# Optimization experiments

Hardware: AMD Instinct MI355X
Metric: run time of the kernel (lower is better)

## Reference

```python
import jax, jax.numpy as jnp
import numpy as np

VOCAB = 21128; EMBED = 768; D_MODEL = 256; H = 100; NTAGS = 21; B = 32; T = 256


def setup_inputs() -> dict:
    key = jax.random.key(0)
    ks = jax.random.split(key, 18)
    n = lambda k, s, sc=0.05: jax.random.normal(k, s, dtype=jnp.float32) * sc
    return {
        "words": jax.random.randint(ks[0], (B, T), 0, VOCAB),
        "target": jax.random.randint(ks[1], (B, T), 0, NTAGS),
        "embed_table": n(ks[2], (VOCAB, EMBED), 1.0),
        "in_fc_w": n(ks[3], (D_MODEL, EMBED)),
        "in_fc_b": n(ks[4], (D_MODEL,)),
        "Wih0": n(ks[5], (2, 4 * H, D_MODEL)),
        "Whh0": n(ks[6], (2, 4 * H, H)),
        "bih0": n(ks[7], (2, 4 * H)),
        "bhh0": n(ks[8], (2, 4 * H)),
        "Wih1": n(ks[9], (2, 4 * H, 2 * H)),
        "Whh1": n(ks[10], (2, 4 * H, H)),
        "bih1": n(ks[11], (2, 4 * H)),
        "bhh1": n(ks[12], (2, 4 * H)),
        "out_w": n(ks[13], (NTAGS, 2 * H)),
        "out_b": n(ks[14], (NTAGS,)),
        "trans": n(ks[15], (NTAGS, NTAGS)),
        "start_s": n(ks[16], (NTAGS,)),
        "end_s": n(ks[17], (NTAGS,)),
    }


def _lstm_dir(x, Wih, Whh, bih, bhh, reverse):
    # x: (T, B, D); torch LSTM gate order i, f, g, o
    Bsz, Hd = x.shape[1], Whh.shape[1]
    pre = jnp.einsum('tbd,gd->tbg', x, Wih) + bih  # precompute input projection

    def step(carry, p):
        h, c = carry
        g = p + h @ Whh.T + bhh
        i, f, gg, o = jnp.split(g, 4, axis=-1)
        c = jax.nn.sigmoid(f) * c + jax.nn.sigmoid(i) * jnp.tanh(gg)
        h = jax.nn.sigmoid(o) * jnp.tanh(c)
        return (h, c), h

    init = (jnp.zeros((Bsz, Hd), x.dtype), jnp.zeros((Bsz, Hd), x.dtype))
    _, hs = jax.lax.scan(step, init, pre, reverse=reverse)
    return hs


def _bilstm(x, layers):
    h = x
    for (Wih, Whh, bih, bhh) in layers:  # fixed small loop over num_layers
        f = _lstm_dir(h, Wih[0], Whh[0], bih[0], bhh[0], False)
        b = _lstm_dir(h, Wih[1], Whh[1], bih[1], bhh[1], True)
        h = jnp.concatenate([f, b], axis=-1)
    return h


def _crf_loss(logits, tags, mask, trans, start_s, end_s):
    # fastNLP ConditionalRandomField loss: normalizer - gold_score, per batch elem
    lt = jnp.swapaxes(logits, 0, 1)          # (T, B, N)
    tt = tags.T                               # (T, B)
    mt = mask.T.astype(logits.dtype)          # (T, B)
    alpha0 = lt[0] + start_s

    def step(alpha, inp):
        emit, m = inp
        tmp = alpha[:, :, None] + trans[None] + emit[:, None, :]  # (B, N, N)
        new = jax.nn.logsumexp(tmp, axis=1)
        return jnp.where(m[:, None] > 0, new, alpha), None

    alpha, _ = jax.lax.scan(step, alpha0, (lt[1:], mt[1:]))
    normalizer = jax.nn.logsumexp(alpha + end_s, axis=1)  # (B,)

    emit_sc = jnp.take_along_axis(lt, tt[..., None], axis=2)[..., 0] * mt
    trans_sc = trans[tt[:-1], tt[1:]] * mt[1:]
    seq_lens = mask.sum(axis=1)
    last_idx = jnp.maximum(seq_lens - 1, 0)
    last_tags = tags[jnp.arange(tags.shape[0]), last_idx]
    gold = emit_sc.sum(0) + trans_sc.sum(0) + start_s[tt[0]] + end_s[last_tags]
    return normalizer - gold


def reference(words, target, embed_table, in_fc_w, in_fc_b, Wih0, Whh0, bih0, bhh0,
              Wih1, Whh1, bih1, bhh1, out_w, out_b, trans, start_s, end_s):
    mask = words != 0
    x = embed_table[words]                       # (B, T, E)
    x = x @ in_fc_w.T + in_fc_b                  # (B, T, D)
    x = jnp.swapaxes(x, 0, 1)                    # (T, B, D)
    h = _bilstm(x, [(Wih0, Whh0, bih0, bhh0), (Wih1, Whh1, bih1, bhh1)])
    h = jnp.swapaxes(h, 0, 1)                    # (B, T, 2H); dropout is identity at eval
    logits = jax.nn.log_softmax(h @ out_w.T + out_b, axis=-1)
    return _crf_loss(logits, target, mask, trans, start_s, end_s)  # (B,)
```

## Files before the change

### kernel.cpp

```cpp
#include <hip/hip_runtime.h>
#include <hip/hip_bf16.h>

#define VOCAB 21128
#define EMBED 768
#define DMODEL 256
#define HID 100
#define NTAGS 21
#define BB 32
#define TT 256
#define NTOK (BB*TT)

typedef float f32x4 __attribute__((ext_vector_type(4)));
typedef unsigned int u32x4 __attribute__((ext_vector_type(4)));
typedef short s16x8 __attribute__((ext_vector_type(8)));

__device__ __forceinline__ float sigm(float x) { return 1.0f / (1.0f + __expf(-x)); }
__device__ __forceinline__ float tanh_(float x) { return 2.0f / (1.0f + __expf(-2.0f * x)) - 1.0f; }

__device__ __forceinline__ unsigned int bfr(float x) {
    unsigned int u = __float_as_uint(x);
    return (u + 0x7fffu + ((u >> 16) & 1u)) >> 16;
}
__device__ __forceinline__ unsigned int bfpack(float lo, float hi) {
    return (bfr(hi) << 16) | bfr(lo);
}
__device__ __forceinline__ s16x8 asfrag(u32x4 v) {
    union { u32x4 u; s16x8 s; } x; x.u = v; return x.s;
}

#define BAR() do { \
    asm volatile("s_waitcnt lgkmcnt(0)" ::: "memory"); \
    __builtin_amdgcn_s_barrier(); \
    __builtin_amdgcn_sched_barrier(0); \
} while (0)

__global__ __launch_bounds__(256) void gemm_mfma(
    const float* __restrict__ A, int lda,
    const float* __restrict__ B, int ldb,
    const float* __restrict__ bias1, const float* __restrict__ bias2,
    float* __restrict__ C, int ldc,
    int N, int K,
    const int* __restrict__ gatherWords, int permGates)
{
    __shared__ unsigned int As_[2][4096];
    __shared__ unsigned int Bs_[2][2048];

    const int tid = threadIdx.x;
    const int row0 = blockIdx.x * 128;
    const int col0 = blockIdx.y * 64;
    const int lane = tid & 63;
    const int wave = tid >> 6;
    const int wr = wave >> 1, wc = wave & 1;
    const int nsteps = (K + 63) >> 6;

    const float* arow[8]; int aoff[8]; int kqA[8];
    #pragma unroll
    for (int j = 0; j < 8; ++j) {
        int v = tid + 256 * j;
        int row = v >> 4, kq = v & 15;
        int grow = row0 + row;
        const float* ap;
        if (gatherWords) {
            int widx = gatherWords[(grow & 31) * TT + (grow >> 5)];
            ap = A + (size_t)widx * lda;
        } else {
            ap = A + (size_t)grow * lda;
        }
        arow[j] = ap + 4 * kq;
        aoff[j] = (row >> 4) * 512 + (kq >> 3) * 256 + ((kq >> 1) & 3) * 64
                + (row & 15) * 4 + (kq & 1) * 2;
        kqA[j] = kq;
    }
    const float* brow[4]; int boff[4]; int bok[4]; int kqB[4];
    #pragma unroll
    for (int j = 0; j < 4; ++j) {
        int v = tid + 256 * j;
        int r = v >> 4, kq = v & 15;
        int gcol = col0 + r;
        bok[j] = (gcol < N);
        int src = bok[j] ? gcol : 0;
        if (permGates && bok[j]) {
            int d2 = (gcol >= 400) ? 1 : 0;
            int rr = gcol - d2 * 400;
            src = d2 * 400 + (rr & 3) * 100 + (rr >> 2);
        }
        brow[j] = B + (size_t)src * ldb + 4 * kq;
        boff[j] = (r >> 4) * 512 + (kq >> 3) * 256 + ((kq >> 1) & 3) * 64
                + (r & 15) * 4 + (kq & 1) * 2;
        kqB[j] = kq;
    }

    {
        #pragma unroll
        for (int j = 0; j < 8; ++j) {
            f32x4 v = {0.f,0.f,0.f,0.f};
            if (4 * kqA[j] < K) v = *(const f32x4*)(arow[j]);
            As_[0][aoff[j]]     = bfpack(v.x, v.y);
            As_[0][aoff[j] + 1] = bfpack(v.z, v.w);
        }
        #pragma unroll
        for (int j = 0; j < 4; ++j) {
            f32x4 v = {0.f,0.f,0.f,0.f};
            if (bok[j] && 4 * kqB[j] < K) v = *(const f32x4*)(brow[j]);
            Bs_[0][boff[j]]     = bfpack(v.x, v.y);
            Bs_[0][boff[j] + 1] = bfpack(v.z, v.w);
        }
    }
    BAR();

    f32x4 acc[4][2] = {};

    for (int s = 0; s < nsteps; ++s) {
        const int cur = s & 1, nxt = cur ^ 1;

        f32x4 la[8], lb[4];
        if (s + 1 < nsteps) {
            const int kb = (s + 1) * 64;
            #pragma unroll
            for (int j = 0; j < 8; ++j) {
                la[j] = (f32x4){0.f,0.f,0.f,0.f};
                if (kb + 4 * kqA[j] < K) la[j] = *(const f32x4*)(arow[j] + kb);
            }
            #pragma unroll
            for (int j = 0; j < 4; ++j) {
                lb[j] = (f32x4){0.f,0.f,0.f,0.f};
                if (bok[j] && kb + 4 * kqB[j] < K) lb[j] = *(const f32x4*)(brow[j] + kb);
            }
        }

        u32x4 af[2][4], bf2[2][2];
        #pragma unroll
        for (int f = 0; f < 2; ++f) {
            #pragma unroll
            for (int mt = 0; mt < 4; ++mt)
                af[f][mt] = *(const u32x4*)&As_[cur][(4 * wr + mt) * 512 + f * 256 + lane * 4];
            #pragma unroll
            for (int nt = 0; nt < 2; ++nt)
                bf2[f][nt] = *(const u32x4*)&Bs_[cur][(2 * wc + nt) * 512 + f * 256 + lane * 4];
        }
        #pragma unroll
        for (int f = 0; f < 2; ++f)
            #pragma unroll
            for (int mt = 0; mt < 4; ++mt)
                #pragma unroll
                for (int nt = 0; nt < 2; ++nt)
                    acc[mt][nt] = __builtin_amdgcn_mfma_f32_16x16x32_bf16(
                        asfrag(af[f][mt]), asfrag(bf2[f][nt]), acc[mt][nt], 0, 0, 0);

        if (s + 1 < nsteps) {
            #pragma unroll
            for (int j = 0; j < 8; ++j) {
                As_[nxt][aoff[j]]     = bfpack(la[j].x, la[j].y);
                As_[nxt][aoff[j] + 1] = bfpack(la[j].z, la[j].w);
            }
            #pragma unroll
            for (int j = 0; j < 4; ++j) {
                Bs_[nxt][boff[j]]     = bfpack(lb[j].x, lb[j].y);
                Bs_[nxt][boff[j] + 1] = bfpack(lb[j].z, lb[j].w);
            }
        }
        BAR();
    }

    const int r4 = (lane >> 4) * 4;
    const int cl = lane & 15;
    #pragma unroll
    for (int nt = 0; nt < 2; ++nt) {
        int gcol = col0 + (2 * wc + nt) * 16 + cl;
        if (gcol < N) {
            int src = gcol;
            if (permGates) {
                int d2 = (gcol >= 400) ? 1 : 0;
                int rr = gcol - d2 * 400;
                src = d2 * 400 + (rr & 3) * 100 + (rr >> 2);
            }
            float bv = bias1[src];
            if (bias2) bv += bias2[src];
            #pragma unroll
            for (int mt = 0; mt < 4; ++mt) {
                int grow = row0 + (4 * wr + mt) * 16 + r4;
                #pragma unroll
                for (int r = 0; r < 4; ++r)
                    C[(size_t)(grow + r) * ldc + gcol] = acc[mt][nt][r] + bv;
            }
        }
    }
}

#define STASH_FRAG(SS, F, A0,A1,A2,A3) { \
    int tile = base + (SS); if (tile > 24) tile = 24; \
    int row16 = 16*tile + m16; \
    const float* srcp = Whh + (size_t)(dir*400 + (row16 & 3)*100 + (row16 >> 2)) * HID; \
    const int k0 = 32*(F) + 8*g4; \
    f32x4 fa = {0.f,0.f,0.f,0.f}, fb = {0.f,0.f,0.f,0.f}; \
    if (k0 < HID) fa = *(const f32x4*)(srcp + k0); \
    if (k0 + 4 < HID) fb = *(const f32x4*)(srcp + k0 + 4); \
    unsigned p0 = bfpack(fa.x, fa.y), p1 = bfpack(fa.z, fa.w); \
    unsigned p2 = bfpack(fb.x, fb.y), p3 = bfpack(fb.z, fb.w); \
    asm volatile("v_accvgpr_write_b32 a" #A0 ", %0\n\t" \
                 "v_accvgpr_write_b32 a" #A1 ", %1\n\t" \
                 "v_accvgpr_write_b32 a" #A2 ", %2\n\t" \
                 "v_accvgpr_write_b32 a" #A3 ", %3" \
                 :: "v"(p0), "v"(p1), "v"(p2), "v"(p3) \
                 : "a" #A0, "a" #A1, "a" #A2, "a" #A3); }

#define MF(ACC, BF, A0, A3) \
    asm volatile("v_mfma_f32_16x16x32_bf16 %0, a[" #A0 ":" #A3 "], %1, %0" \
                 : "+v"(ACC) : "v"(BF));

#define LOADCHUNK(K2) { \
    const int s0_ = 16 * (K2); \
    _Pragma("unroll") \
    for (int j = 0; j < 7; ++j) { \
        if (okj[j]) { \
            int tg = dir ? (TT - 1 - (s0_ + sicj[j])) : (s0_ + sicj[j]); \
            rr[j] = *(const f32x4*)(pre + (size_t)(tg * BB + b) * 800 + dir * 400 + 4 * gqj[j]); \
        } \
    } }

#define WRITECHUNK(BUF) { \
    _Pragma("unroll") \
    for (int j = 0; j < 7; ++j) { \
        if (okj[j]) *(f32x4*)&preS[(BUF) * 6400 + sicj[j] * 400 + 4 * gqj[j]] = rr[j]; \
    } }

#define LSTM_STEP(SIC) { \
    const int t_ = dir ? (TT - 1 - (s0 + (SIC))) : (s0 + (SIC)); \
    const int i_ = t_ * BB + b; \
    const u32x4* hb_ = (const u32x4*)&h16[(SIC) & 1][0]; \
    u32x4 bf0 = hb_[g4], bf1 = hb_[4+g4], bf2 = hb_[8+g4], bf3 = hb_[12+g4]; \
    f32x4 p4 = *(const f32x4*)&preS[curbase + (SIC) * 400 + my_po]; \
    f32x4 acc0 = {0.f,0.f,0.f,0.f}, acc1 = {0.f,0.f,0.f,0.f}; \
    f32x4 acc2 = {0.f,0.f,0.f,0.f}, acc3 = {0.f,0.f,0.f,0.f}; \
    f32x4 acc4 = {0.f,0.f,0.f,0.f}, acc5 = {0.f,0.f,0.f,0.f}; \
    f32x4 acc6 = {0.f,0.f,0.f,0.f}; \
    asm volatile("s_nop 1"); \
    MF(acc0, bf0, 0, 3)    MF(acc1, bf0, 16, 19)  MF(acc2, bf0, 32, 35) \
    MF(acc3, bf0, 48, 51)  MF(acc4, bf0, 64, 67)  MF(acc5, bf0, 80, 83) \
    MF(acc6, bf0, 96, 99) \
    MF(acc0, bf1, 4, 7)    MF(acc1, bf1, 20, 23)  MF(acc2, bf1, 36, 39) \
    MF(acc3, bf1, 52, 55)  MF(acc4, bf1, 68, 71)  MF(acc5, bf1, 84, 87) \
    MF(acc6, bf1, 100, 103) \
    MF(acc0, bf2, 8, 11)   MF(acc1, bf2, 24, 27)  MF(acc2, bf2, 40, 43) \
    MF(acc3, bf2, 56, 59)  MF(acc4, bf2, 72, 75)  MF(acc5, bf2, 88, 91) \
    MF(acc6, bf2, 104, 107) \
    MF(acc0, bf3, 12, 15)  MF(acc1, bf3, 28, 31)  MF(acc2, bf3, 44, 47) \
    MF(acc3, bf3, 60, 63)  MF(acc4, bf3, 76, 79)  MF(acc5, bf3, 92, 95) \
    MF(acc6, bf3, 108, 111) \
    asm volatile("s_nop 7\n\ts_nop 7"); \
    f32x4 t01 = (slot_sel & 1) ? acc1 : acc0; \
    f32x4 t23 = (slot_sel & 1) ? acc3 : acc2; \
    f32x4 t45 = (slot_sel & 1) ? acc5 : acc4; \
    f32x4 u0 = (slot_sel & 2) ? t23 : t01; \
    f32x4 u1 = (slot_sel & 2) ? acc6 : t45; \
    f32x4 sel = (slot_sel & 4) ? u1 : u0; \
    float igt = sigm(sel.x + p4.x); \
    float fgt = sigm(sel.y + p4.y); \
    float ggt = tanh_(sel.z + p4.z); \
    float ogt = sigm(sel.w + p4.w); \
    c = fgt * c + igt * ggt; \
    float h = ogt * tanh_(c); \
    if (writer) { \
        h16[((SIC) + 1) & 1][my_u] = (unsigned short)bfr(h); \
        hout[(size_t)i_ * 200 + dir * HID + my_u] = h; \
    } \
    BAR(); }

__global__ __launch_bounds__(256, 1) void lstm_mfma(
    const float* __restrict__ pre,
    const float* __restrict__ Whh,
    float* __restrict__ hout)
{
    const int dir = blockIdx.x >> 5;
    const int b = blockIdx.x & 31;
    const int tid = threadIdx.x;
    const int wave = tid >> 6;
    const int lane = tid & 63;
    const int m16 = lane & 15;
    const int g4 = lane >> 4;
    const int slot_sel = lane & 7;

    const int base = (wave == 0) ? 0 : (wave == 1) ? 7 : (wave == 2) ? 13 : 19;

    __shared__ alignas(16) unsigned short h16[2][128];
    __shared__ alignas(16) float preS[2 * 6400];

    STASH_FRAG(0,0, 0,1,2,3)      STASH_FRAG(0,1, 4,5,6,7)
    STASH_FRAG(0,2, 8,9,10,11)    STASH_FRAG(0,3, 12,13,14,15)
    STASH_FRAG(1,0, 16,17,18,19)  STASH_FRAG(1,1, 20,21,22,23)
    STASH_FRAG(1,2, 24,25,26,27)  STASH_FRAG(1,3, 28,29,30,31)
    STASH_FRAG(2,0, 32,33,34,35)  STASH_FRAG(2,1, 36,37,38,39)
    STASH_FRAG(2,2, 40,41,42,43)  STASH_FRAG(2,3, 44,45,46,47)
    STASH_FRAG(3,0, 48,49,50,51)  STASH_FRAG(3,1, 52,53,54,55)
    STASH_FRAG(3,2, 56,57,58,59)  STASH_FRAG(3,3, 60,61,62,63)
    STASH_FRAG(4,0, 64,65,66,67)  STASH_FRAG(4,1, 68,69,70,71)
    STASH_FRAG(4,2, 72,73,74,75)  STASH_FRAG(4,3, 76,77,78,79)
    STASH_FRAG(5,0, 80,81,82,83)  STASH_FRAG(5,1, 84,85,86,87)
    STASH_FRAG(5,2, 88,89,90,91)  STASH_FRAG(5,3, 92,93,94,95)
    STASH_FRAG(6,0, 96,97,98,99)  STASH_FRAG(6,1, 100,101,102,103)
    STASH_FRAG(6,2, 104,105,106,107) STASH_FRAG(6,3, 108,109,110,111)

    if (tid < 128) { h16[0][tid] = 0; h16[1][tid] = 0; }

    int my_tile = base + ((slot_sel < 7) ? slot_sel : 6);
    if (my_tile > 24) my_tile = 24;
    const int my_u = 4 * my_tile + g4;
    const int my_po = 16 * my_tile + 4 * g4;
    const int ow_lim = (wave == 0) ? 7 : 6;
    const bool writer = (slot_sel < ow_lim) && ((lane & 8) == 0);

    int sicj[7], gqj[7]; bool okj[7];
    #pragma unroll
    for (int j = 0; j < 7; ++j) {
        int idx = tid + 256 * j;
        okj[j] = (idx < 1600);
        int ic = okj[j] ? idx : 0;
        sicj[j] = ic / 100;
        gqj[j] = ic - 100 * sicj[j];
    }

    float c = 0.f;
    f32x4 rr[7];

    LOADCHUNK(0)
    WRITECHUNK(0)
    LOADCHUNK(1)
    BAR();

    for (int k = 0; k < 16; ++k) {
        const int s0 = 16 * k;
        const int curbase = (k & 1) * 6400;
        LSTM_STEP(0)  LSTM_STEP(1)  LSTM_STEP(2)  LSTM_STEP(3)
        LSTM_STEP(4)  LSTM_STEP(5)  LSTM_STEP(6)  LSTM_STEP(7)
        LSTM_STEP(8)  LSTM_STEP(9)  LSTM_STEP(10) LSTM_STEP(11)
        LSTM_STEP(12) LSTM_STEP(13) LSTM_STEP(14) LSTM_STEP(15)
        if (k < 15) { WRITECHUNK((k & 1) ^ 1) }
        if (k < 14) { LOADCHUNK(k + 2) }
        BAR();
    }
}

__global__ __launch_bounds__(256) void logits_lsm(
    const float* __restrict__ h1,
    const float* __restrict__ out_w,
    const float* __restrict__ out_b,
    float* __restrict__ logits)
{
    const int lane = threadIdx.x & 63;
    const int wid = (blockIdx.x * 256 + threadIdx.x) >> 6;
    const int half = lane >> 5;
    const int n = lane & 31;
    const int i = wid * 2 + half;
    if (i >= NTOK) return;

    float acc = -1e30f;
    if (n < NTAGS) {
        acc = out_b[n];
        const float4* hr = (const float4*)(h1 + (size_t)i * 200);
        const float4* wr = (const float4*)(out_w + (size_t)n * 200);
        #pragma unroll
        for (int e = 0; e < 50; ++e) {
            float4 h4 = hr[e], w4 = wr[e];
            acc += h4.x * w4.x + h4.y * w4.y + h4.z * w4.z + h4.w * w4.w;
        }
    }
    float m = acc;
    for (int off = 16; off > 0; off >>= 1) m = fmaxf(m, __shfl_xor(m, off, 32));
    float ex = (n < NTAGS) ? __expf(acc - m) : 0.f;
    float s = ex;
    for (int off = 16; off > 0; off >>= 1) s += __shfl_xor(s, off, 32);
    if (n < NTAGS) logits[(size_t)i * NTAGS + n] = acc - m - __logf(s);
}

__global__ __launch_bounds__(64) void crf_kernel(
    const float* __restrict__ logits,
    const int* __restrict__ words,
    const int* __restrict__ target,
    const float* __restrict__ trans,
    const float* __restrict__ start_s,
    const float* __restrict__ end_s,
    float* __restrict__ out)
{
    const int b = blockIdx.x;
    const int j = threadIdx.x;
    const int j21 = (j < NTAGS) ? j : (NTAGS - 1);

    float tcol[NTAGS];
    #pragma unroll
    for (int i = 0; i < NTAGS; ++i) tcol[i] = (j < NTAGS) ? trans[i * NTAGS + j] : 0.f;

    const int w0 = words[b * TT +   0 + j];
    const int w1 = words[b * TT +  64 + j];
    const int w2 = words[b * TT + 128 + j];
    const int w3 = words[b * TT + 192 + j];

    float alpha = (j < NTAGS) ? (logits[(size_t)(0 * BB + b) * NTAGS + j] + start_s[j]) : -1e30f;
    float e_cur = logits[(size_t)(1 * BB + b) * NTAGS + j21];

#define CRF_CHUNK(WREG, T0) \
    for (int u = ((T0) == 0 ? 1 : 0); u < 64; ++u) { \
        const int t = (T0) + u; \
        float e_nxt = 0.f; \
        if (t + 1 < TT) e_nxt = logits[(size_t)((t + 1) * BB + b) * NTAGS + j21]; \
        if (__shfl(WREG, u, 64) != 0) { \
            float v[NTAGS]; \
            _Pragma("unroll") \
            for (int i2 = 0; i2 < NTAGS; ++i2) \
                v[i2] = __shfl(alpha, i2, 64) + tcol[i2]; \
            float m0[11]; \
            _Pragma("unroll") \
            for (int p = 0; p < 10; ++p) m0[p] = fmaxf(v[2*p], v[2*p+1]); \
            m0[10] = v[20]; \
            float m1[6]; \
            _Pragma("unroll") \
            for (int p = 0; p < 5; ++p) m1[p] = fmaxf(m0[2*p], m0[2*p+1]); \
            m1[5] = m0[10]; \
            float m2a = fmaxf(m1[0], m1[1]), m2b = fmaxf(m1[2], m1[3]), m2c = fmaxf(m1[4], m1[5]); \
            float mx = fmaxf(fmaxf(m2a, m2b), m2c); \
            float e[NTAGS]; \
            _Pragma("unroll") \
            for (int i2 = 0; i2 < NTAGS; ++i2) e[i2] = __expf(v[i2] - mx); \
            float s0[11]; \
            _Pragma("unroll") \
            for (int p = 0; p < 10; ++p) s0[p] = e[2*p] + e[2*p+1]; \
            s0[10] = e[20]; \
            float s1[6]; \
            _Pragma("unroll") \
            for (int p = 0; p < 5; ++p) s1[p] = s0[2*p] + s0[2*p+1]; \
            s1[5] = s0[10]; \
            float ss = ((s1[0] + s1[1]) + (s1[2] + s1[3])) + (s1[4] + s1[5]); \
            float na = mx + __logf(ss) + e_cur; \
            alpha = (j < NTAGS) ? na : -1e30f; \
        } \
        e_cur = e_nxt; \
    }

    CRF_CHUNK(w0, 0)
    CRF_CHUNK(w1, 64)
    CRF_CHUNK(w2, 128)
    CRF_CHUNK(w3, 192)
#undef CRF_CHUNK

    float val = (j < NTAGS) ? (alpha + end_s[j]) : -1e30f;
    float mx = val;
    for (int off = 32; off > 0; off >>= 1) mx = fmaxf(mx, __shfl_xor(mx, off, 64));
    float s = (j < NTAGS) ? __expf(val - mx) : 0.f;
    for (int off = 32; off > 0; off >>= 1) s += __shfl_xor(s, off, 64);
    float norm = mx + __logf(s);

    float gold = 0.f, slen = 0.f;
    for (int t = j; t < TT; t += 64) {
        int tg = target[b * TT + t];
        bool m = (words[b * TT + t] != 0);
        if (m) {
            gold += logits[(size_t)(t * BB + b) * NTAGS + tg];
            slen += 1.f;
            if (t >= 1) gold += trans[target[b * TT + t - 1] * NTAGS + tg];
        }
    }
    for (int off = 32; off > 0; off >>= 1) {
        gold += __shfl_xor(gold, off, 64);
        slen += __shfl_xor(slen, off, 64);
    }
    if (j == 0) {
        int len = (int)slen;
        int last = (len > 0) ? (len - 1) : 0;
        int last_tag = target[b * TT + last];
        gold += start_s[target[b * TT + 0]] + end_s[last_tag];
        out[b] = norm - gold;
    }
}

extern "C" void kernel_launch(void* const* d_in, const int* in_sizes, int n_in,
                              void* d_out, int out_size, void* d_ws, size_t ws_size,
                              hipStream_t stream) {
    const int*   words   = (const int*)  d_in[0];
    const int*   target  = (const int*)  d_in[1];
    const float* embed   = (const float*)d_in[2];
    const float* in_fc_w = (const float*)d_in[3];
    const float* in_fc_b = (const float*)d_in[4];
    const float* Wih0    = (const float*)d_in[5];
    const float* Whh0    = (const float*)d_in[6];
    const float* bih0    = (const float*)d_in[7];
    const float* bhh0    = (const float*)d_in[8];
    const float* Wih1    = (const float*)d_in[9];
    const float* Whh1    = (const float*)d_in[10];
    const float* bih1    = (const float*)d_in[11];
    const float* bhh1    = (const float*)d_in[12];
    const float* out_w   = (const float*)d_in[13];
    const float* out_b   = (const float*)d_in[14];
    const float* trans   = (const float*)d_in[15];
    const float* start_s = (const float*)d_in[16];
    const float* end_s   = (const float*)d_in[17];
    float* out = (float*)d_out;

    float* ws = (float*)d_ws;
    float* x      = ws;
    float* pre    = ws + 2097152;
    float* h0     = ws + 8650752;
    float* h1     = ws;
    float* logits = ws + 1638400;

    gemm_mfma<<<dim3(64, 4), 256, 0, stream>>>(
        embed, EMBED, in_fc_w, EMBED, in_fc_b, nullptr,
        x, DMODEL, DMODEL, EMBED, words, 0);

    gemm_mfma<<<dim3(64, 13), 256, 0, stream>>>(
        x, DMODEL, Wih0, DMODEL, bih0, bhh0,
        pre, 800, 800, DMODEL, nullptr, 1);

    lstm_mfma<<<64, 256, 0, stream>>>(pre, Whh0, h0);

    gemm_mfma<<<dim3(64, 13), 256, 0, stream>>>(
        h0, 200, Wih1, 200, bih1, bhh1,
        pre, 800, 800, 200, nullptr, 1);

    lstm_mfma<<<64, 256, 0, stream>>>(pre, Whh1, h1);

    logits_lsm<<<NTOK / 8, 256, 0, stream>>>(h1, out_w, out_b, logits);

    crf_kernel<<<BB, 64, 0, stream>>>(logits, words, target, trans, start_s, end_s, out);
}
```

Measured before the change: 559.9 us.

## Run both LSTM directions in one 512-thread block per batch element

The recurrent LSTM kernel now launches one 512-thread block per batch element, with waves 0-3 handling the forward direction and waves 4-7 the backward direction. Each direction gets its own slices of the shared hidden-state and preactivation buffers. To fit the shared-memory budget, the staged chunk shrinks from 16 to 8 timesteps, with twice as many chunk iterations. The aim is to halve the block count and share a CU between directions, but every step's barrier now synchronises eight waves that do not depend on each other, and refill points come twice as often.

```diff
diff --git a/kernel.cpp b/kernel.cpp
--- a/kernel.cpp
+++ b/kernel.cpp
@@ -209,9 +209,9 @@
                  : "+v"(ACC) : "v"(BF));
 
 #define LOADCHUNK(K2) { \
-    const int s0_ = 16 * (K2); \
+    const int s0_ = 8 * (K2); \
     _Pragma("unroll") \
-    for (int j = 0; j < 7; ++j) { \
+    for (int j = 0; j < 4; ++j) { \
         if (okj[j]) { \
             int tg = dir ? (TT - 1 - (s0_ + sicj[j])) : (s0_ + sicj[j]); \
             rr[j] = *(const f32x4*)(pre + (size_t)(tg * BB + b) * 800 + dir * 400 + 4 * gqj[j]); \
@@ -220,16 +220,16 @@
 
 #define WRITECHUNK(BUF) { \
     _Pragma("unroll") \
-    for (int j = 0; j < 7; ++j) { \
-        if (okj[j]) *(f32x4*)&preS[(BUF) * 6400 + sicj[j] * 400 + 4 * gqj[j]] = rr[j]; \
+    for (int j = 0; j < 4; ++j) { \
+        if (okj[j]) *(f32x4*)&preS[dir][(BUF) * 3200 + sicj[j] * 400 + 4 * gqj[j]] = rr[j]; \
     } }
 
 #define LSTM_STEP(SIC) { \
     const int t_ = dir ? (TT - 1 - (s0 + (SIC))) : (s0 + (SIC)); \
     const int i_ = t_ * BB + b; \
-    const u32x4* hb_ = (const u32x4*)&h16[(SIC) & 1][0]; \
+    const u32x4* hb_ = (const u32x4*)&h16[dir][(SIC) & 1][0]; \
     u32x4 bf0 = hb_[g4], bf1 = hb_[4+g4], bf2 = hb_[8+g4], bf3 = hb_[12+g4]; \
-    f32x4 p4 = *(const f32x4*)&preS[curbase + (SIC) * 400 + my_po]; \
+    f32x4 p4 = *(const f32x4*)&preS[dir][curbase + (SIC) * 400 + my_po]; \
     f32x4 acc0 = {0.f,0.f,0.f,0.f}, acc1 = {0.f,0.f,0.f,0.f}; \
     f32x4 acc2 = {0.f,0.f,0.f,0.f}, acc3 = {0.f,0.f,0.f,0.f}; \
     f32x4 acc4 = {0.f,0.f,0.f,0.f}, acc5 = {0.f,0.f,0.f,0.f}; \
@@ -261,29 +261,31 @@
     c = fgt * c + igt * ggt; \
     float h = ogt * tanh_(c); \
     if (writer) { \
-        h16[((SIC) + 1) & 1][my_u] = (unsigned short)bfr(h); \
+        h16[dir][((SIC) + 1) & 1][my_u] = (unsigned short)bfr(h); \
         hout[(size_t)i_ * 200 + dir * HID + my_u] = h; \
     } \
     BAR(); }
 
-__global__ __launch_bounds__(256, 1) void lstm_mfma(
+__global__ __launch_bounds__(512, 1) void lstm_mfma(
     const float* __restrict__ pre,
     const float* __restrict__ Whh,
     float* __restrict__ hout)
 {
-    const int dir = blockIdx.x >> 5;
-    const int b = blockIdx.x & 31;
+    const int b = blockIdx.x;
     const int tid = threadIdx.x;
     const int wave = tid >> 6;
+    const int dir = wave >> 2;
+    const int wavel = wave & 3;
     const int lane = tid & 63;
     const int m16 = lane & 15;
     const int g4 = lane >> 4;
     const int slot_sel = lane & 7;
-
-    const int base = (wave == 0) ? 0 : (wave == 1) ? 7 : (wave == 2) ? 13 : 19;
-
-    __shared__ alignas(16) unsigned short h16[2][128];
-    __shared__ alignas(16) float preS[2 * 6400];
+    const int tidl = tid & 255;
+
+    const int base = (wavel == 0) ? 0 : (wavel == 1) ? 7 : (wavel == 2) ? 13 : 19;
+
+    __shared__ alignas(16) unsigned short h16[2][2][128];
+    __shared__ alignas(16) float preS[2][6400];
 
     STASH_FRAG(0,0, 0,1,2,3)      STASH_FRAG(0,1, 4,5,6,7)
     STASH_FRAG(0,2, 8,9,10,11)    STASH_FRAG(0,3, 12,13,14,15)
@@ -300,42 +302,43 @@
     STASH_FRAG(6,0, 96,97,98,99)  STASH_FRAG(6,1, 100,101,102,103)
     STASH_FRAG(6,2, 104,105,106,107) STASH_FRAG(6,3, 108,109,110,111)
 
-    if (tid < 128) { h16[0][tid] = 0; h16[1][tid] = 0; }
+    if (tid < 512) {
+        unsigned short* hz = (unsigned short*)h16;
+        if (tid < 2 * 2 * 128) hz[tid] = 0;
+    }
 
     int my_tile = base + ((slot_sel < 7) ? slot_sel : 6);
     if (my_tile > 24) my_tile = 24;
     const int my_u = 4 * my_tile + g4;
     const int my_po = 16 * my_tile + 4 * g4;
-    const int ow_lim = (wave == 0) ? 7 : 6;
+    const int ow_lim = (wavel == 0) ? 7 : 6;
     const bool writer = (slot_sel < ow_lim) && ((lane & 8) == 0);
 
-    int sicj[7], gqj[7]; bool okj[7];
+    int sicj[4], gqj[4]; bool okj[4];
     #pragma unroll
-    for (int j = 0; j < 7; ++j) {
-        int idx = tid + 256 * j;
-        okj[j] = (idx < 1600);
+    for (int j = 0; j < 4; ++j) {
+        int idx = tidl + 256 * j;
+        okj[j] = (idx < 800);
         int ic = okj[j] ? idx : 0;
         sicj[j] = ic / 100;
         gqj[j] = ic - 100 * sicj[j];
     }
 
     float c = 0.f;
-    f32x4 rr[7];
+    f32x4 rr[4];
 
     LOADCHUNK(0)
     WRITECHUNK(0)
     LOADCHUNK(1)
     BAR();
 
-    for (int k = 0; k < 16; ++k) {
-        const int s0 = 16 * k;
-        const int curbase = (k & 1) * 6400;
+    for (int k = 0; k < 32; ++k) {
+        const int s0 = 8 * k;
+        const int curbase = (k & 1) * 3200;
         LSTM_STEP(0)  LSTM_STEP(1)  LSTM_STEP(2)  LSTM_STEP(3)
         LSTM_STEP(4)  LSTM_STEP(5)  LSTM_STEP(6)  LSTM_STEP(7)
-        LSTM_STEP(8)  LSTM_STEP(9)  LSTM_STEP(10) LSTM_STEP(11)
-        LSTM_STEP(12) LSTM_STEP(13) LSTM_STEP(14) LSTM_STEP(15)
-        if (k < 15) { WRITECHUNK((k & 1) ^ 1) }
-        if (k < 14) { LOADCHUNK(k + 2) }
+        if (k < 31) { WRITECHUNK((k & 1) ^ 1) }
+        if (k < 30) { LOADCHUNK(k + 2) }
         BAR();
     }
 }
@@ -509,13 +512,13 @@
         x, DMODEL, Wih0, DMODEL, bih0, bhh0,
         pre, 800, 800, DMODEL, nullptr, 1);
 
-    lstm_mfma<<<64, 256, 0, stream>>>(pre, Whh0, h0);
+    lstm_mfma<<<32, 512, 0, stream>>>(pre, Whh0, h0);
 
     gemm_mfma<<<dim3(64, 13), 256, 0, stream>>>(
         h0, 200, Wih1, 200, bih1, bhh1,
         pre, 800, 800, 200, nullptr, 1);
 
-    lstm_mfma<<<64, 256, 0, stream>>>(pre, Whh1, h1);
+    lstm_mfma<<<32, 512, 0, stream>>>(pre, Whh1, h1);
 
     logits_lsm<<<NTOK / 8, 256, 0, stream>>>(h1, out_w, out_b, logits);
 
```

Measured after the change: 713.4 us. +27.4%, slower.
